# Kernel optimization log

Hardware: AMD Instinct MI355X
Metric: run time of the kernel (lower is better)

Reference implementation:

```python
import jax, jax.numpy as jnp
import numpy as np

N_NODES = 100000
N_EDGES = 1600000
NFEAT, NHID, NCLASS = 128, 64, 16


def gcn_conv(x, W, edge_index, edge_weight, num_nodes):
    # PyG GCNConv (normalize=False, add_self_loops=False, bias=False):
    # h = x @ W ; out[i] = sum over edges (j->i) of edge_weight * h[j]
    h = x @ W                                  # [N, out]
    src, dst = edge_index[0], edge_index[1]
    msgs = h[src] * edge_weight[:, None]       # [E, out] gathered messages
    return jax.ops.segment_sum(msgs, dst, num_segments=num_nodes)


def setup_inputs() -> dict:
    key = jax.random.key(0)
    k = jax.random.split(key, 7)
    x = jax.random.normal(k[0], (N_NODES, NFEAT), dtype=jnp.float32)
    edge_index1 = jax.random.randint(k[1], (2, N_EDGES), 0, N_NODES, dtype=jnp.int32)
    edge_index2 = jax.random.randint(k[2], (2, N_EDGES), 0, N_NODES, dtype=jnp.int32)
    edge_weight1 = jax.random.uniform(k[3], (N_EDGES,), dtype=jnp.float32)
    edge_weight2 = jax.random.uniform(k[4], (N_EDGES,), dtype=jnp.float32)
    # Glorot-style linear weights (GCNConv lin, bias=False)
    W1 = jax.random.normal(k[5], (NFEAT, NHID), dtype=jnp.float32) / np.sqrt(NFEAT)
    W2 = jax.random.normal(k[6], (NHID, NCLASS), dtype=jnp.float32) / np.sqrt(NHID)
    return {"x": x, "edge_index1": edge_index1, "edge_index2": edge_index2,
            "edge_weight1": edge_weight1, "edge_weight2": edge_weight2,
            "W1": W1, "W2": W2}


def reference(x, edge_index1, edge_index2, edge_weight1, edge_weight2, W1, W2):
    n = x.shape[0]
    h = jax.nn.relu(gcn_conv(x, W1, edge_index1, edge_weight1, n))
    out = gcn_conv(h, W2, edge_index2, edge_weight2, n)
    return out
```

## Files before the change

kernel.cpp:

```cpp
#include <hip/hip_runtime.h>
#include <hip/hip_bf16.h>


#define EPB 4096
#define NBMAX 512
#define CAP 6144

__global__ __launch_bounds__(256) void gemm1_hist_kernel(
        const float* __restrict__ x, const float* __restrict__ W1,
        __hip_bfloat16* __restrict__ h1,
        const int* __restrict__ ei1, const int* __restrict__ ei2,
        int* __restrict__ hist_g, int n_nodes, int n_edges, int nblk, int nb,
        int gemm_blocks) {
    __shared__ float As[32][132];
    __shared__ float Bs[32][64];
    __shared__ int hist[NBMAX];
    int tid = threadIdx.x;

    if (blockIdx.x < gemm_blocks) {
        int node0 = blockIdx.x * 128;
        int n4 = (tid & 31) * 4;
        int f8 = (tid >> 5) * 8;
        float acc[4][8];
#pragma unroll
        for (int i = 0; i < 4; ++i)
#pragma unroll
            for (int j = 0; j < 8; ++j) acc[i][j] = 0.f;

        const float4* x4 = reinterpret_cast<const float4*>(x);
        const float4* W4 = reinterpret_cast<const float4*>(W1);

        for (int s = 0; s < 4; ++s) {
#pragma unroll
            for (int j = 0; j < 4; ++j) {
                int idx = tid + j * 256;
                int n = idx >> 3;
                int kq = idx & 7;
                float4 v = make_float4(0.f, 0.f, 0.f, 0.f);
                if (node0 + n < n_nodes) v = x4[(size_t)(node0 + n) * 32 + s * 8 + kq];
                int k4 = kq * 4;
                As[k4 + 0][n] = v.x;
                As[k4 + 1][n] = v.y;
                As[k4 + 2][n] = v.z;
                As[k4 + 3][n] = v.w;
            }
#pragma unroll
            for (int j = 0; j < 2; ++j) {
                int idx = tid + j * 256;
                int k = idx >> 4;
                int fq = idx & 15;
                *reinterpret_cast<float4*>(&Bs[k][fq * 4]) = W4[(size_t)(s * 32 + k) * 16 + fq];
            }
            __syncthreads();
#pragma unroll
            for (int kk = 0; kk < 32; ++kk) {
                float4 a = *reinterpret_cast<const float4*>(&As[kk][n4]);
                float4 b0 = *reinterpret_cast<const float4*>(&Bs[kk][f8]);
                float4 b1 = *reinterpret_cast<const float4*>(&Bs[kk][f8 + 4]);
                float av[4] = {a.x, a.y, a.z, a.w};
                float bv[8] = {b0.x, b0.y, b0.z, b0.w, b1.x, b1.y, b1.z, b1.w};
#pragma unroll
                for (int i = 0; i < 4; ++i)
#pragma unroll
                    for (int j = 0; j < 8; ++j) acc[i][j] += av[i] * bv[j];
            }
            __syncthreads();
        }
#pragma unroll
        for (int i = 0; i < 4; ++i) {
            int n = node0 + n4 + i;
            if (n < n_nodes) {
                __hip_bfloat16 tmp[8];
#pragma unroll
                for (int j = 0; j < 8; ++j) tmp[j] = __float2bfloat16(acc[i][j]);
                *reinterpret_cast<uint4*>(&h1[(size_t)n * 64 + f8]) =
                    *reinterpret_cast<const uint4*>(tmp);
            }
        }
    } else {
        int blk = blockIdx.x - gemm_blocks;
        int layer = (blk >= nblk) ? 1 : 0;
        int lblk = blk - layer * nblk;
        const int* ei = layer ? ei2 : ei1;
        for (int i = tid; i < nb; i += 256) hist[i] = 0;
        __syncthreads();
        int e0 = lblk * EPB;
#pragma unroll
        for (int j = 0; j < EPB / 256; ++j) {
            int e = e0 + tid + j * 256;
            if (e < n_edges) atomicAdd(&hist[ei[n_edges + e] >> 8], 1);
        }
        __syncthreads();
        int base = layer * nb * nblk;
        for (int i = tid; i < nb; i += 256) hist_g[base + i * nblk + lblk] = hist[i];
    }
}

__global__ void scan_local_k(int* __restrict__ data, int* __restrict__ bsums, int n) {
    __shared__ int tmp[1024];
    int i = blockIdx.x * 1024 + threadIdx.x;
    int v = (i < n) ? data[i] : 0;
    tmp[threadIdx.x] = v;
    __syncthreads();
    for (int off = 1; off < 1024; off <<= 1) {
        int t = (threadIdx.x >= off) ? tmp[threadIdx.x - off] : 0;
        __syncthreads();
        tmp[threadIdx.x] += t;
        __syncthreads();
    }
    if (i < n) data[i] = tmp[threadIdx.x] - v;
    if (threadIdx.x == 1023) bsums[blockIdx.x] = tmp[1023];
}

__global__ void scan_top_k(int* __restrict__ bsums, int nbk) {
    __shared__ int tmp[512];
    int v = (threadIdx.x < nbk) ? bsums[threadIdx.x] : 0;
    tmp[threadIdx.x] = v;
    __syncthreads();
    for (int off = 1; off < 512; off <<= 1) {
        int t = (threadIdx.x >= off) ? tmp[threadIdx.x - off] : 0;
        __syncthreads();
        tmp[threadIdx.x] += t;
        __syncthreads();
    }
    if (threadIdx.x < nbk) bsums[threadIdx.x] = tmp[threadIdx.x] - v;
}

__global__ void add_offsets_k(int* __restrict__ data, const int* __restrict__ bsums, int n) {
    int i = blockIdx.x * 1024 + threadIdx.x;
    if (i < n) data[i] += bsums[blockIdx.x];
}

__global__ void bin_scatter_kernel(const int* __restrict__ ei1, const int* __restrict__ ei2,
                                   const float* __restrict__ ew1, const float* __restrict__ ew2,
                                   const int* __restrict__ scan_g, int2* __restrict__ rec_out,
                                   int n_edges, int nblk, int nb) {
    __shared__ int2 srec[EPB];
    __shared__ unsigned short sbkt[EPB];
    __shared__ int loff[NBMAX], cur[NBMAX], gbase[NBMAX];
    __shared__ int p[256];
    int tid = threadIdx.x, blk = blockIdx.x;
    int layer = (blk >= nblk) ? 1 : 0;
    int lblk = blk - layer * nblk;
    const int* ei = layer ? ei2 : ei1;
    const float* ew = layer ? ew2 : ew1;
    int n_scan_tot = 2 * nb * nblk;
    int total = 2 * n_edges;
    int base = layer * nb * nblk;
    int e0 = lblk * EPB;
    int cnt = min(EPB, n_edges - e0);
    for (int i = tid; i < nb; i += 256) {
        int l = base + i * nblk + lblk;
        int g = scan_g[l];
        int nxt = (l + 1 < n_scan_tot) ? scan_g[l + 1] : total;
        gbase[i] = g;
        loff[i] = nxt - g;
    }
    __syncthreads();
    int b0 = tid * 2;
    int c0 = (b0 < nb) ? loff[b0] : 0;
    int c1 = (b0 + 1 < nb) ? loff[b0 + 1] : 0;
    p[tid] = c0 + c1;
    __syncthreads();
    for (int off = 1; off < 256; off <<= 1) {
        int t = (tid >= off) ? p[tid - off] : 0;
        __syncthreads();
        p[tid] += t;
        __syncthreads();
    }
    int pbase = (tid > 0) ? p[tid - 1] : 0;
    __syncthreads();
    if (b0 < nb)     { loff[b0] = pbase;          cur[b0] = pbase; }
    if (b0 + 1 < nb) { loff[b0 + 1] = pbase + c0; cur[b0 + 1] = pbase + c0; }
    __syncthreads();
#pragma unroll
    for (int j = 0; j < EPB / 256; ++j) {
        int e = e0 + tid + j * 256;
        if (e < n_edges) {
            int s = ei[e], d = ei[n_edges + e];
            int b = d >> 8;
            int r = atomicAdd(&cur[b], 1);
            srec[r] = make_int2(s | ((d & 255) << 20), __float_as_int(ew[e]));
            sbkt[r] = (unsigned short)b;
        }
    }
    __syncthreads();
    for (int i = tid; i < cnt; i += 256) {
        int b = sbkt[i];
        rec_out[gbase[b] + (i - loff[b])] = srec[i];
    }
}


__global__ __launch_bounds__(256) void bucket_sort_kernel(
        const int2* __restrict__ rec_in, const int* __restrict__ scan_g,
        int2* __restrict__ rec_out, int* __restrict__ rowptr1, int* __restrict__ rowptr2,
        int n_nodes, int n_edges, int nblk, int nb) {
    __shared__ int2 srec[CAP];
    __shared__ int hist[256], cur[256], rp[256];
    int tid = threadIdx.x, b = blockIdx.x;
    int layer = (b >= nb) ? 1 : 0;
    int lb = b - layer * nb;
    int* rowptr = layer ? rowptr2 : rowptr1;
    int sh = layer ? 6 : 7;
    int total = 2 * n_edges;
    int start = scan_g[b * nblk];
    int end = (b + 1 < 2 * nb) ? scan_g[(b + 1) * nblk] : total;
    int cnt = end - start;
    hist[tid] = 0;
    __syncthreads();
    for (int i = tid; i < cnt; i += 256) {
        int2 r = rec_in[start + i];
        atomicAdd(&hist[(r.x >> 20) & 255], 1);
    }
    __syncthreads();
    int v = hist[tid];
    rp[tid] = v;
    __syncthreads();
    for (int off = 1; off < 256; off <<= 1) {
        int t = (tid >= off) ? rp[tid - off] : 0;
        __syncthreads();
        rp[tid] += t;
        __syncthreads();
    }
    int excl = rp[tid] - v;
    cur[tid] = excl;
    int node = (lb << 8) + tid;
    if (node < n_nodes) rowptr[node] = start + excl;
    if (lb == nb - 1 && tid == 0) rowptr[n_nodes] = end;
    __syncthreads();
    for (int i = tid; i < cnt; i += 256) {
        int2 r = rec_in[start + i];
        int rk = atomicAdd(&cur[(r.x >> 20) & 255], 1);
        r.x = (r.x & 0xFFFFF) << sh;
        if (rk < CAP) srec[rk] = r;
    }
    __syncthreads();
    int lim = min(cnt, CAP);
    for (int i = tid; i < lim; i += 256) rec_out[start + i] = srec[i];
}


#define G1_EDGE(rr, aa) \
    aa += __bfloat162float(*(const __hip_bfloat16*)(h1b + (unsigned)(rr).x + f2)) * \
          __int_as_float((rr).y)

__global__ __launch_bounds__(256) void gather1_kernel(const __hip_bfloat16* __restrict__ h1,
                                                      const int* __restrict__ rowptr,
                                                      const int2* __restrict__ rec,
                                                      const float* __restrict__ W2,
                                                      float* __restrict__ h2, int n_nodes) {
    int tid = threadIdx.x;
    int w = tid >> 6, f = tid & 63;
    unsigned f2 = (unsigned)(f << 1);
    const char* h1b = (const char*)h1;
    int n = blockIdx.x * 4 + w;
    bool valid = (n < n_nodes);
    int i = 0, end = 0;
    if (valid) { i = rowptr[n]; end = rowptr[n + 1]; }
    float a0 = 0.f, a1 = 0.f, a2 = 0.f, a3 = 0.f;
    float a4 = 0.f, a5 = 0.f, a6 = 0.f, a7 = 0.f;
    float a8 = 0.f, a9 = 0.f, a10 = 0.f, a11 = 0.f;
    float a12 = 0.f, a13 = 0.f, a14 = 0.f, a15 = 0.f;
    for (; i + 15 < end; i += 16) {
        int2 r0 = rec[i],      r1 = rec[i + 1],  r2 = rec[i + 2],  r3 = rec[i + 3];
        int2 r4 = rec[i + 4],  r5 = rec[i + 5],  r6 = rec[i + 6],  r7 = rec[i + 7];
        int2 r8 = rec[i + 8],  r9 = rec[i + 9],  r10 = rec[i + 10], r11 = rec[i + 11];
        int2 r12 = rec[i + 12], r13 = rec[i + 13], r14 = rec[i + 14], r15 = rec[i + 15];
        G1_EDGE(r0, a0);   G1_EDGE(r1, a1);   G1_EDGE(r2, a2);   G1_EDGE(r3, a3);
        G1_EDGE(r4, a4);   G1_EDGE(r5, a5);   G1_EDGE(r6, a6);   G1_EDGE(r7, a7);
        G1_EDGE(r8, a8);   G1_EDGE(r9, a9);   G1_EDGE(r10, a10); G1_EDGE(r11, a11);
        G1_EDGE(r12, a12); G1_EDGE(r13, a13); G1_EDGE(r14, a14); G1_EDGE(r15, a15);
    }
    for (; i + 7 < end; i += 8) {
        int2 r0 = rec[i],     r1 = rec[i + 1], r2 = rec[i + 2], r3 = rec[i + 3];
        int2 r4 = rec[i + 4], r5 = rec[i + 5], r6 = rec[i + 6], r7 = rec[i + 7];
        G1_EDGE(r0, a0); G1_EDGE(r1, a1); G1_EDGE(r2, a2); G1_EDGE(r3, a3);
        G1_EDGE(r4, a4); G1_EDGE(r5, a5); G1_EDGE(r6, a6); G1_EDGE(r7, a7);
    }
    for (; i + 3 < end; i += 4) {
        int2 r0 = rec[i], r1 = rec[i + 1], r2 = rec[i + 2], r3 = rec[i + 3];
        G1_EDGE(r0, a0); G1_EDGE(r1, a1); G1_EDGE(r2, a2); G1_EDGE(r3, a3);
    }
    for (; i < end; ++i) {
        int2 r = rec[i];
        G1_EDGE(r, a0);
    }
    float s0 = ((a0 + a1) + (a2 + a3)) + ((a4 + a5) + (a6 + a7));
    float s1 = ((a8 + a9) + (a10 + a11)) + ((a12 + a13) + (a14 + a15));
    float r = fmaxf(s0 + s1, 0.f);
    int c = f & 15, kq = f >> 4;
    float pacc = 0.f;
#pragma unroll
    for (int j = 0; j < 16; ++j) {
        int k = kq * 16 + j;
        float rk = __shfl(r, k, 64);
        pacc += rk * W2[k * 16 + c];
    }
    pacc += __shfl_xor(pacc, 16, 64);
    pacc += __shfl_xor(pacc, 32, 64);
    if (valid && f < 16) h2[(size_t)n * 16 + f] = pacc;
}


#define G2_EDGE(rr, aa) \
    aa += *(const float*)(h2b + (unsigned)(rr).x + f4) * __int_as_float((rr).y)

__global__ void gather2_kernel(const float* __restrict__ h2,
                               const int* __restrict__ rowptr,
                               const int2* __restrict__ rec,
                               float* __restrict__ out, int n_nodes) {
    int n = blockIdx.x * 16 + (threadIdx.x >> 4);
    if (n >= n_nodes) return;
    int f = threadIdx.x & 15;
    unsigned f4 = (unsigned)(f << 2);
    const char* h2b = (const char*)h2;
    int i = rowptr[n], end = rowptr[n + 1];
    float a0 = 0.f, a1 = 0.f, a2 = 0.f, a3 = 0.f;
    float a4 = 0.f, a5 = 0.f, a6 = 0.f, a7 = 0.f;
    for (; i + 7 < end; i += 8) {
        int2 r0 = rec[i],     r1 = rec[i + 1], r2 = rec[i + 2], r3 = rec[i + 3];
        int2 r4 = rec[i + 4], r5 = rec[i + 5], r6 = rec[i + 6], r7 = rec[i + 7];
        G2_EDGE(r0, a0); G2_EDGE(r1, a1); G2_EDGE(r2, a2); G2_EDGE(r3, a3);
        G2_EDGE(r4, a4); G2_EDGE(r5, a5); G2_EDGE(r6, a6); G2_EDGE(r7, a7);
    }
    for (; i + 3 < end; i += 4) {
        int2 r0 = rec[i], r1 = rec[i + 1], r2 = rec[i + 2], r3 = rec[i + 3];
        G2_EDGE(r0, a0); G2_EDGE(r1, a1); G2_EDGE(r2, a2); G2_EDGE(r3, a3);
    }
    for (; i < end; ++i) {
        int2 r = rec[i];
        G2_EDGE(r, a0);
    }
    out[(size_t)n * 16 + f] = (((a0 + a1) + (a2 + a3)) + ((a4 + a5) + (a6 + a7)));
}


extern "C" void kernel_launch(void* const* d_in, const int* in_sizes, int n_in,
                              void* d_out, int out_size, void* d_ws, size_t ws_size,
                              hipStream_t stream) {
    const float* x   = (const float*)d_in[0];
    const int*   ei1 = (const int*)d_in[1];
    const int*   ei2 = (const int*)d_in[2];
    const float* ew1 = (const float*)d_in[3];
    const float* ew2 = (const float*)d_in[4];
    const float* W1  = (const float*)d_in[5];
    const float* W2  = (const float*)d_in[6];

    const int n_nodes = in_sizes[0] / 128;
    const int n_edges = in_sizes[1] / 2;
    const int nb   = (n_nodes + 255) >> 8;
    const int nblk = (n_edges + EPB - 1) / EPB;
    const int n_scan_tot = 2 * nb * nblk;
    const int scan_blocks = (n_scan_tot + 1023) / 1024;
    const int gemm_blocks = (n_nodes + 127) / 128;

    int2* rec2   = (int2*)d_ws;
    int2* recbuf = rec2 + (size_t)2 * n_edges;
    int*  hist_g = (int*)(recbuf + (size_t)2 * n_edges);
    int*  bsums  = hist_g + n_scan_tot;
    int*  rowptr1 = bsums + 512;
    int*  rowptr2 = rowptr1 + n_nodes + 1;
    __hip_bfloat16* h1 = (__hip_bfloat16*)(rowptr2 + n_nodes + 1);
    float* h2 = (float*)recbuf;
    float* out = (float*)d_out;

    gemm1_hist_kernel<<<gemm_blocks + 2 * nblk, 256, 0, stream>>>(
        x, W1, h1, ei1, ei2, hist_g, n_nodes, n_edges, nblk, nb, gemm_blocks);
    scan_local_k<<<scan_blocks, 1024, 0, stream>>>(hist_g, bsums, n_scan_tot);
    scan_top_k<<<1, 512, 0, stream>>>(bsums, scan_blocks);
    add_offsets_k<<<scan_blocks, 1024, 0, stream>>>(hist_g, bsums, n_scan_tot);
    bin_scatter_kernel<<<2 * nblk, 256, 0, stream>>>(ei1, ei2, ew1, ew2, hist_g, recbuf,
                                                     n_edges, nblk, nb);
    bucket_sort_kernel<<<2 * nb, 256, 0, stream>>>(recbuf, hist_g, rec2, rowptr1, rowptr2,
                                                   n_nodes, n_edges, nblk, nb);

    gather1_kernel<<<(n_nodes + 3) / 4, 256, 0, stream>>>(h1, rowptr1, rec2, W2, h2, n_nodes);
    gather2_kernel<<<(n_nodes + 15) / 16, 256, 0, stream>>>(h2, rowptr2, rec2, out, n_nodes);
}
```

Measured before the change: 297.8 us.

## Fold top-level scan into consumers and enlarge GEMM1 tile to 256 nodes

Removes the scan_top_k and add_offsets_k launches. bin_scatter and bucket_sort now each rescan the per-block sums in shared memory and add the offset when they read the histogram scan. This cuts two kernel launches and one pass over the histogram, at the cost of a redundant small scan in every block of the two consumers. The GEMM1 tile also doubles to 256 nodes by 16 features per thread, which raises per-thread register use and LDS size in exchange for more reuse per load.

```diff
diff --git a/kernel.cpp b/kernel.cpp
--- a/kernel.cpp
+++ b/kernel.cpp
@@ -12,27 +12,27 @@
         const int* __restrict__ ei1, const int* __restrict__ ei2,
         int* __restrict__ hist_g, int n_nodes, int n_edges, int nblk, int nb,
         int gemm_blocks) {
-    __shared__ float As[32][132];
+    __shared__ float As[32][260];
     __shared__ float Bs[32][64];
     __shared__ int hist[NBMAX];
     int tid = threadIdx.x;
 
     if (blockIdx.x < gemm_blocks) {
-        int node0 = blockIdx.x * 128;
-        int n4 = (tid & 31) * 4;
-        int f8 = (tid >> 5) * 8;
-        float acc[4][8];
+        int node0 = blockIdx.x * 256;
+        int n4 = (tid & 63) * 4;
+        int f16 = (tid >> 6) * 16;
+        float acc[4][16];
 #pragma unroll
         for (int i = 0; i < 4; ++i)
 #pragma unroll
-            for (int j = 0; j < 8; ++j) acc[i][j] = 0.f;
+            for (int j = 0; j < 16; ++j) acc[i][j] = 0.f;
 
         const float4* x4 = reinterpret_cast<const float4*>(x);
         const float4* W4 = reinterpret_cast<const float4*>(W1);
 
         for (int s = 0; s < 4; ++s) {
 #pragma unroll
-            for (int j = 0; j < 4; ++j) {
+            for (int j = 0; j < 8; ++j) {
                 int idx = tid + j * 256;
                 int n = idx >> 3;
                 int kq = idx & 7;
@@ -54,15 +54,18 @@
             __syncthreads();
 #pragma unroll
             for (int kk = 0; kk < 32; ++kk) {
-                float4 a = *reinterpret_cast<const float4*>(&As[kk][n4]);
-                float4 b0 = *reinterpret_cast<const float4*>(&Bs[kk][f8]);
-                float4 b1 = *reinterpret_cast<const float4*>(&Bs[kk][f8 + 4]);
+                float4 a  = *reinterpret_cast<const float4*>(&As[kk][n4]);
+                float4 b0 = *reinterpret_cast<const float4*>(&Bs[kk][f16]);
+                float4 b1 = *reinterpret_cast<const float4*>(&Bs[kk][f16 + 4]);
+                float4 b2 = *reinterpret_cast<const float4*>(&Bs[kk][f16 + 8]);
+                float4 b3 = *reinterpret_cast<const float4*>(&Bs[kk][f16 + 12]);
                 float av[4] = {a.x, a.y, a.z, a.w};
-                float bv[8] = {b0.x, b0.y, b0.z, b0.w, b1.x, b1.y, b1.z, b1.w};
+                float bv[16] = {b0.x, b0.y, b0.z, b0.w, b1.x, b1.y, b1.z, b1.w,
+                                b2.x, b2.y, b2.z, b2.w, b3.x, b3.y, b3.z, b3.w};
 #pragma unroll
                 for (int i = 0; i < 4; ++i)
 #pragma unroll
-                    for (int j = 0; j < 8; ++j) acc[i][j] += av[i] * bv[j];
+                    for (int j = 0; j < 16; ++j) acc[i][j] += av[i] * bv[j];
             }
             __syncthreads();
         }
@@ -70,11 +73,13 @@
         for (int i = 0; i < 4; ++i) {
             int n = node0 + n4 + i;
             if (n < n_nodes) {
-                __hip_bfloat16 tmp[8];
-#pragma unroll
-                for (int j = 0; j < 8; ++j) tmp[j] = __float2bfloat16(acc[i][j]);
-                *reinterpret_cast<uint4*>(&h1[(size_t)n * 64 + f8]) =
-                    *reinterpret_cast<const uint4*>(tmp);
+                __hip_bfloat16 tmp[16];
+#pragma unroll
+                for (int j = 0; j < 16; ++j) tmp[j] = __float2bfloat16(acc[i][j]);
+                *reinterpret_cast<uint4*>(&h1[(size_t)n * 64 + f16]) =
+                    *reinterpret_cast<const uint4*>(&tmp[0]);
+                *reinterpret_cast<uint4*>(&h1[(size_t)n * 64 + f16 + 8]) =
+                    *reinterpret_cast<const uint4*>(&tmp[8]);
             }
         }
     } else {
@@ -112,33 +117,16 @@
     if (threadIdx.x == 1023) bsums[blockIdx.x] = tmp[1023];
 }
 
-__global__ void scan_top_k(int* __restrict__ bsums, int nbk) {
-    __shared__ int tmp[512];
-    int v = (threadIdx.x < nbk) ? bsums[threadIdx.x] : 0;
-    tmp[threadIdx.x] = v;
-    __syncthreads();
-    for (int off = 1; off < 512; off <<= 1) {
-        int t = (threadIdx.x >= off) ? tmp[threadIdx.x - off] : 0;
-        __syncthreads();
-        tmp[threadIdx.x] += t;
-        __syncthreads();
-    }
-    if (threadIdx.x < nbk) bsums[threadIdx.x] = tmp[threadIdx.x] - v;
-}
-
-__global__ void add_offsets_k(int* __restrict__ data, const int* __restrict__ bsums, int n) {
-    int i = blockIdx.x * 1024 + threadIdx.x;
-    if (i < n) data[i] += bsums[blockIdx.x];
-}
-
 __global__ void bin_scatter_kernel(const int* __restrict__ ei1, const int* __restrict__ ei2,
                                    const float* __restrict__ ew1, const float* __restrict__ ew2,
-                                   const int* __restrict__ scan_g, int2* __restrict__ rec_out,
-                                   int n_edges, int nblk, int nb) {
+                                   const int* __restrict__ scan_g, const int* __restrict__ bsums,
+                                   int2* __restrict__ rec_out,
+                                   int n_edges, int nblk, int nb, int nbk) {
     __shared__ int2 srec[EPB];
     __shared__ unsigned short sbkt[EPB];
     __shared__ int loff[NBMAX], cur[NBMAX], gbase[NBMAX];
     __shared__ int p[256];
+    __shared__ int bscan[512];
     int tid = threadIdx.x, blk = blockIdx.x;
     int layer = (blk >= nblk) ? 1 : 0;
     int lblk = blk - layer * nblk;
@@ -149,10 +137,29 @@
     int base = layer * nb * nblk;
     int e0 = lblk * EPB;
     int cnt = min(EPB, n_edges - e0);
+
+    {
+        int t2 = tid * 2;
+        int v0 = (t2 < nbk) ? bsums[t2] : 0;
+        int v1 = (t2 + 1 < nbk) ? bsums[t2 + 1] : 0;
+        p[tid] = v0 + v1;
+        __syncthreads();
+        for (int off = 1; off < 256; off <<= 1) {
+            int t = (tid >= off) ? p[tid - off] : 0;
+            __syncthreads();
+            p[tid] += t;
+            __syncthreads();
+        }
+        int pb = (tid > 0) ? p[tid - 1] : 0;
+        bscan[t2] = pb;
+        bscan[t2 + 1] = pb + v0;
+        __syncthreads();
+    }
+
     for (int i = tid; i < nb; i += 256) {
         int l = base + i * nblk + lblk;
-        int g = scan_g[l];
-        int nxt = (l + 1 < n_scan_tot) ? scan_g[l + 1] : total;
+        int g = scan_g[l] + bscan[l >> 10];
+        int nxt = (l + 1 < n_scan_tot) ? (scan_g[l + 1] + bscan[(l + 1) >> 10]) : total;
         gbase[i] = g;
         loff[i] = nxt - g;
     }
@@ -194,18 +201,41 @@
 
 __global__ __launch_bounds__(256) void bucket_sort_kernel(
         const int2* __restrict__ rec_in, const int* __restrict__ scan_g,
+        const int* __restrict__ bsums,
         int2* __restrict__ rec_out, int* __restrict__ rowptr1, int* __restrict__ rowptr2,
-        int n_nodes, int n_edges, int nblk, int nb) {
+        int n_nodes, int n_edges, int nblk, int nb, int nbk) {
     __shared__ int2 srec[CAP];
-    __shared__ int hist[256], cur[256], rp[256];
+    __shared__ int hist[256], cur[256], rp[256], p[256];
+    __shared__ int bscan[512];
     int tid = threadIdx.x, b = blockIdx.x;
     int layer = (b >= nb) ? 1 : 0;
     int lb = b - layer * nb;
     int* rowptr = layer ? rowptr2 : rowptr1;
     int sh = layer ? 6 : 7;
     int total = 2 * n_edges;
-    int start = scan_g[b * nblk];
-    int end = (b + 1 < 2 * nb) ? scan_g[(b + 1) * nblk] : total;
+
+    {
+        int t2 = tid * 2;
+        int v0 = (t2 < nbk) ? bsums[t2] : 0;
+        int v1 = (t2 + 1 < nbk) ? bsums[t2 + 1] : 0;
+        p[tid] = v0 + v1;
+        __syncthreads();
+        for (int off = 1; off < 256; off <<= 1) {
+            int t = (tid >= off) ? p[tid - off] : 0;
+            __syncthreads();
+            p[tid] += t;
+            __syncthreads();
+        }
+        int pb = (tid > 0) ? p[tid - 1] : 0;
+        bscan[t2] = pb;
+        bscan[t2 + 1] = pb + v0;
+        __syncthreads();
+    }
+
+    int l0 = b * nblk;
+    int start = scan_g[l0] + bscan[l0 >> 10];
+    int l1 = (b + 1) * nblk;
+    int end = (b + 1 < 2 * nb) ? (scan_g[l1] + bscan[l1 >> 10]) : total;
     int cnt = end - start;
     hist[tid] = 0;
     __syncthreads();
@@ -353,7 +383,7 @@
     const int nblk = (n_edges + EPB - 1) / EPB;
     const int n_scan_tot = 2 * nb * nblk;
     const int scan_blocks = (n_scan_tot + 1023) / 1024;
-    const int gemm_blocks = (n_nodes + 127) / 128;
+    const int gemm_blocks = (n_nodes + 255) / 256;
 
     int2* rec2   = (int2*)d_ws;
     int2* recbuf = rec2 + (size_t)2 * n_edges;
@@ -368,12 +398,11 @@
     gemm1_hist_kernel<<<gemm_blocks + 2 * nblk, 256, 0, stream>>>(
         x, W1, h1, ei1, ei2, hist_g, n_nodes, n_edges, nblk, nb, gemm_blocks);
     scan_local_k<<<scan_blocks, 1024, 0, stream>>>(hist_g, bsums, n_scan_tot);
-    scan_top_k<<<1, 512, 0, stream>>>(bsums, scan_blocks);
-    add_offsets_k<<<scan_blocks, 1024, 0, stream>>>(hist_g, bsums, n_scan_tot);
-    bin_scatter_kernel<<<2 * nblk, 256, 0, stream>>>(ei1, ei2, ew1, ew2, hist_g, recbuf,
-                                                     n_edges, nblk, nb);
-    bucket_sort_kernel<<<2 * nb, 256, 0, stream>>>(recbuf, hist_g, rec2, rowptr1, rowptr2,
-                                                   n_nodes, n_edges, nblk, nb);
+    bin_scatter_kernel<<<2 * nblk, 256, 0, stream>>>(ei1, ei2, ew1, ew2, hist_g, bsums,
+                                                     recbuf, n_edges, nblk, nb, scan_blocks);
+    bucket_sort_kernel<<<2 * nb, 256, 0, stream>>>(recbuf, hist_g, bsums, rec2,
+                                                   rowptr1, rowptr2,
+                                                   n_nodes, n_edges, nblk, nb, scan_blocks);
 
     gather1_kernel<<<(n_nodes + 3) / 4, 256, 0, stream>>>(h1, rowptr1, rec2, W2, h2, n_nodes);
     gather2_kernel<<<(n_nodes + 15) / 16, 256, 0, stream>>>(h2, rowptr2, rec2, out, n_nodes);
```

Result: slower. 349.1 us (+17.2%).
